# Kernel optimization log

Hardware: AMD Instinct MI355X
Metric: run time of the kernel (lower is better)

Reference implementation:

```python
import jax, jax.numpy as jnp
import numpy as np

N = 100000
E = 1000000
D_IN = 64
H1, C1 = 12, 12   # conv1: heads=12, out=12 -> concat 144
H2, C2 = 1, 64    # conv2: heads=1, out=64
NEG_SLOPE = 0.2
ALPHA = 0.5       # SSGConv alpha, K=1


def setup_inputs() -> dict:
    key = jax.random.key(0)
    ks = jax.random.split(key, 16)
    features = jax.random.normal(ks[0], (N, D_IN), dtype=jnp.float32)
    # edges with no self loops (PyG GATv2 removes then re-adds self loops)
    src = jax.random.randint(ks[1], (E,), 0, N)
    off = jax.random.randint(ks[2], (E,), 1, N)
    dst = (src + off) % N
    edge_index = jnp.stack([src, dst]).astype(jnp.int64)
    g = lambda k, shape, fan: (jax.random.normal(k, shape, jnp.float32) * (1.0 / np.sqrt(fan)))
    params = dict(
        W_ssg=g(ks[3], (D_IN, D_IN), D_IN), b_ssg=jnp.zeros((D_IN,), jnp.float32),
        W1l=g(ks[4], (D_IN, H1 * C1), D_IN), b1l=jnp.zeros((H1 * C1,), jnp.float32),
        W1r=g(ks[5], (D_IN, H1 * C1), D_IN), b1r=jnp.zeros((H1 * C1,), jnp.float32),
        att1=g(ks[6], (H1, C1), C1), bias1=jnp.zeros((H1 * C1,), jnp.float32),
        W2l=g(ks[7], (H1 * C1, H2 * C2), H1 * C1), b2l=jnp.zeros((H2 * C2,), jnp.float32),
        W2r=g(ks[8], (H1 * C1, H2 * C2), H1 * C1), b2r=jnp.zeros((H2 * C2,), jnp.float32),
        att2=g(ks[9], (H2, C2), C2), bias2=jnp.zeros((H2 * C2,), jnp.float32),
    )
    return dict(features=features, edge_index=edge_index, **params)


def _add_self_loops(src, dst):
    loop = jnp.arange(N, dtype=src.dtype)
    return jnp.concatenate([src, loop]), jnp.concatenate([dst, loop])


def _ssg_conv(x, src, dst, W, b):
    # gcn_norm with self loops, edge weight 1
    s, d = _add_self_loops(src, dst)
    deg = jax.ops.segment_sum(jnp.ones_like(s, dtype=x.dtype), d, num_segments=N)
    dinv = jnp.where(deg > 0, jax.lax.rsqrt(deg), 0.0)
    norm = dinv[s] * dinv[d]                      # [E+N]
    agg = jax.ops.segment_sum(x[s] * norm[:, None], d, num_segments=N)
    h = ALPHA * x + (1.0 - ALPHA) * agg           # K=1
    return h @ W + b


def _gatv2_conv(x, src, dst, Wl, bl, Wr, br, att, bias, Hh, Cc):
    s, d = _add_self_loops(src, dst)
    xl = (x @ Wl + bl).reshape(N, Hh, Cc)
    xr = (x @ Wr + br).reshape(N, Hh, Cc)
    e = jax.nn.leaky_relu(xl[s] + xr[d], NEG_SLOPE)       # [E', H, C]
    logits = jnp.einsum('ehc,hc->eh', e, att)             # [E', H]
    m = jax.ops.segment_max(logits, d, num_segments=N)    # [N, H]
    a = jnp.exp(logits - m[d])
    denom = jax.ops.segment_sum(a, d, num_segments=N)
    a = a / (denom[d] + 1e-16)                            # segment softmax
    out = jax.ops.segment_sum(xl[s] * a[:, :, None], d, num_segments=N)
    return out.reshape(N, Hh * Cc) + bias


def reference(features, edge_index, W_ssg, b_ssg, W1l, b1l, W1r, b1r,
              att1, bias1, W2l, b2l, W2r, b2r, att2, bias2):
    src, dst = edge_index[0], edge_index[1]
    x = _ssg_conv(features, src, dst, W_ssg, b_ssg)
    x = _gatv2_conv(x, src, dst, W1l, b1l, W1r, b1r, att1, bias1, H1, C1)
    x = _gatv2_conv(x, src, dst, W2l, b2l, W2r, b2r, att2, bias2, H2, C2)
    return x
```

## Files before the change

### kernel.cpp

```cpp
#include <hip/hip_runtime.h>

#define NNODE 100000
#define NEDGE 1000000
#define CAP 64

typedef __attribute__((ext_vector_type(4))) float f32x4;
typedef __attribute__((ext_vector_type(8))) short bf16x8;

__device__ __forceinline__ float lrelu(float x){ return x >= 0.f ? x : 0.2f*x; }
__device__ __forceinline__ unsigned short f2bf(float f){
    unsigned u = __float_as_uint(f);
    unsigned r = (u + 0x7FFFu + ((u >> 16) & 1u)) >> 16;
    return (unsigned short)r;
}
__device__ __forceinline__ float bf2f(unsigned short h){
    return __uint_as_float(((unsigned)h) << 16);
}

__global__ void detect_kernel(const int* __restrict__ ei, int* __restrict__ flag){
    int t = threadIdx.x;
    int nz = ei[2*t + 1];
    unsigned long long b = __ballot(nz != 0);
    if (t == 0) flag[0] = (b == 0ULL) ? 1 : 0;
}

__global__ __launch_bounds__(256) void scatter_kernel(const int* __restrict__ ei,
                                                      const int* __restrict__ flag,
                                                      int* __restrict__ cnt,
                                                      int* __restrict__ col){
    int e = blockIdx.x * 256 + threadIdx.x;
    if (e >= NEDGE) return;
    int s, d;
    if (flag[0]){ s = ei[2*e]; d = ei[2*(NEDGE + e)]; }
    else        { s = ei[e];   d = ei[NEDGE + e]; }
    if ((unsigned)s < NNODE && (unsigned)d < NNODE){
        int p = atomicAdd(&cnt[d], 1);
        if (p < CAP) col[d*CAP + p] = s;
    }
}

__global__ __launch_bounds__(256) void setup_kernel(const int* __restrict__ cnt,
                                                    float* __restrict__ dinv,
                                                    const float* __restrict__ Wssg,
                                                    const float* __restrict__ bssg,
                                                    const float* __restrict__ W1l,
                                                    const float* __restrict__ b1l,
                                                    const float* __restrict__ W1r,
                                                    const float* __restrict__ b1r,
                                                    unsigned short* __restrict__ Wct,
                                                    float* __restrict__ bc,
                                                    const float* __restrict__ W2l,
                                                    const float* __restrict__ b2l,
                                                    const float* __restrict__ W2r,
                                                    const float* __restrict__ b2r,
                                                    unsigned short* __restrict__ W2t,
                                                    float* __restrict__ b2c){
    int b = blockIdx.x;
    if (b < 391){
        int i = b * 256 + threadIdx.x;
        if (i < NNODE) dinv[i] = rsqrtf((float)(cnt[i] + 1));
    } else if (b < 463){
        int id = (b - 391) * 256 + threadIdx.x;
        if (id < 2*64*144){
            int which = id / (64*144);
            int rem = id - which*64*144;
            int k = rem / 144, j = rem - (rem/144)*144;
            const float* W1 = which ? W1r : W1l;
            float s = 0.f;
            #pragma unroll 8
            for (int c = 0; c < 64; ++c)
                s = fmaf(Wssg[k*64 + c], W1[c*144 + j], s);
            Wct[(size_t)(which*144 + j)*64 + k] = f2bf(s);
        }
        if (id < 2*144){
            int which = id / 144, j = id - which*144;
            const float* W1 = which ? W1r : W1l;
            const float* b1 = which ? b1r : b1l;
            float s = b1[j];
            #pragma unroll 8
            for (int c = 0; c < 64; ++c)
                s = fmaf(bssg[c], W1[c*144 + j], s);
            bc[which*144 + j] = s;
        }
    } else {
        int id = (b - 463) * 256 + threadIdx.x;
        if (id < 128*160){
            int j = id / 160, k = id - (id/160)*160;
            float v = 0.f;
            if (k < 144) v = (j < 64) ? W2l[k*64 + j] : W2r[k*64 + (j - 64)];
            W2t[(size_t)j*160 + k] = f2bf(v);
        }
        if (id < 128) b2c[id] = (id < 64) ? b2l[id] : b2r[id - 64];
    }
}

__global__ __launch_bounds__(256) void ssg_kernel(const float* __restrict__ x,
                                                  const int* __restrict__ col,
                                                  const int* __restrict__ cnt,
                                                  const float* __restrict__ dinv,
                                                  unsigned short* __restrict__ hb){
    int wid = threadIdx.x >> 6, lane = threadIdx.x & 63;
    int d = blockIdx.x * 4 + wid;
    int cq = lane & 7, eq = lane >> 3;
    float di = dinv[d];
    int deg = min(cnt[d], CAP);
    int myc = (lane < deg) ? col[d*CAP + lane] : 0;
    float wl = (lane < deg) ? dinv[myc] : 0.f;
    float a0=0.f,a1=0.f,a2=0.f,a3=0.f,a4=0.f,a5=0.f,a6=0.f,a7=0.f;
    for (int e0 = 0; e0 < deg; e0 += 8){
        int e = e0 + eq;
        bool val = e < deg;
        int idx = val ? e : 0;
        int se = __shfl(myc, idx);
        float w = __shfl(wl, idx);
        if (!val) w = 0.f;
        float4 v0 = *(const float4*)&x[(size_t)se*64 + 8*cq];
        float4 v1 = *(const float4*)&x[(size_t)se*64 + 8*cq + 4];
        a0 = fmaf(w, v0.x, a0); a1 = fmaf(w, v0.y, a1);
        a2 = fmaf(w, v0.z, a2); a3 = fmaf(w, v0.w, a3);
        a4 = fmaf(w, v1.x, a4); a5 = fmaf(w, v1.y, a5);
        a6 = fmaf(w, v1.z, a6); a7 = fmaf(w, v1.w, a7);
    }
    #pragma unroll
    for (int m = 8; m < 64; m <<= 1){
        a0 += __shfl_xor(a0, m); a1 += __shfl_xor(a1, m);
        a2 += __shfl_xor(a2, m); a3 += __shfl_xor(a3, m);
        a4 += __shfl_xor(a4, m); a5 += __shfl_xor(a5, m);
        a6 += __shfl_xor(a6, m); a7 += __shfl_xor(a7, m);
    }
    if (eq == 0){
        float4 xd0 = *(const float4*)&x[(size_t)d*64 + 8*cq];
        float4 xd1 = *(const float4*)&x[(size_t)d*64 + 8*cq + 4];
        float dd = di*di;
        ushort4 o0, o1;
        o0.x = f2bf(0.5f*xd0.x + 0.5f*fmaf(di, a0, dd*xd0.x));
        o0.y = f2bf(0.5f*xd0.y + 0.5f*fmaf(di, a1, dd*xd0.y));
        o0.z = f2bf(0.5f*xd0.z + 0.5f*fmaf(di, a2, dd*xd0.z));
        o0.w = f2bf(0.5f*xd0.w + 0.5f*fmaf(di, a3, dd*xd0.w));
        o1.x = f2bf(0.5f*xd1.x + 0.5f*fmaf(di, a4, dd*xd1.x));
        o1.y = f2bf(0.5f*xd1.y + 0.5f*fmaf(di, a5, dd*xd1.y));
        o1.z = f2bf(0.5f*xd1.z + 0.5f*fmaf(di, a6, dd*xd1.z));
        o1.w = f2bf(0.5f*xd1.w + 0.5f*fmaf(di, a7, dd*xd1.w));
        *(ushort4*)&hb[(size_t)d*64 + 8*cq]     = o0;
        *(ushort4*)&hb[(size_t)d*64 + 8*cq + 4] = o1;
    }
}

template<int K, int OUT1, int OUT2>
__global__ __launch_bounds__(256) void gemm_mfma_kernel(const unsigned short* __restrict__ Xb,
                                                        const unsigned short* __restrict__ Wt,
                                                        const float* __restrict__ Bc,
                                                        unsigned short* __restrict__ Y1,
                                                        unsigned short* __restrict__ Y2){
    constexpr int OUT = OUT1 + OUT2;
    constexpr int NT = OUT / 16;
    int wid = threadIdx.x >> 6, lane = threadIdx.x & 63;
    int m = lane & 15, kg = lane >> 4;
    int row0 = blockIdx.x * 64 + wid * 16;
    int rA = row0 + m; if (rA > NNODE-1) rA = NNODE-1;
    f32x4 acc[NT];
    #pragma unroll
    for (int t = 0; t < NT; ++t) acc[t] = (f32x4){0.f, 0.f, 0.f, 0.f};
    #pragma unroll
    for (int k0 = 0; k0 < K; k0 += 32){
        bf16x8 a = *(const bf16x8*)&Xb[(size_t)rA*K + k0 + 8*kg];
        #pragma unroll
        for (int t = 0; t < NT; ++t){
            bf16x8 b = *(const bf16x8*)&Wt[(size_t)(t*16 + m)*K + k0 + 8*kg];
            acc[t] = __builtin_amdgcn_mfma_f32_16x16x32_bf16(a, b, acc[t], 0, 0, 0);
        }
    }
    int rbase = row0 + 4*kg;
    #pragma unroll
    for (int t = 0; t < NT; ++t){
        int colg = t*16 + m;
        float bias = Bc[colg];
        #pragma unroll
        for (int r = 0; r < 4; ++r){
            int gr = rbase + r;
            if (gr < NNODE){
                unsigned short v = f2bf(acc[t][r] + bias);
                if (colg < OUT1) Y1[(size_t)gr*OUT1 + colg] = v;
                else             Y2[(size_t)gr*OUT2 + (colg - OUT1)] = v;
            }
        }
    }
}

__global__ __launch_bounds__(192) void gat1_kernel(const unsigned short* __restrict__ xl,
                                                   const unsigned short* __restrict__ xr,
                                                   const int* __restrict__ col,
                                                   const int* __restrict__ cnt,
                                                   const float* __restrict__ att,
                                                   const float* __restrict__ bias,
                                                   unsigned short* __restrict__ xg){
    __shared__ __align__(16) float V[16][148];
    __shared__ float A[16][13];
    __shared__ __align__(16) float P[4][36][4];
    __shared__ float Lp[4][12];
    __shared__ int scol[65];
    int d = blockIdx.x, t = threadIdx.x;
    int deg = min(cnt[d], CAP);
    int ne = deg + 1;
    if (t < deg) scol[t] = col[d*CAP + t];
    if (t == deg) scol[t] = d;
    int h = t % 12;
    int eslot = t / 12;
    float xrr[12], attr[12];
    {
        const ushort4* xrp = (const ushort4*)&xr[(size_t)d*144 + h*12];
        ushort4 q0 = xrp[0], q1 = xrp[1], q2 = xrp[2];
        xrr[0]=bf2f(q0.x); xrr[1]=bf2f(q0.y); xrr[2]=bf2f(q0.z); xrr[3]=bf2f(q0.w);
        xrr[4]=bf2f(q1.x); xrr[5]=bf2f(q1.y); xrr[6]=bf2f(q1.z); xrr[7]=bf2f(q1.w);
        xrr[8]=bf2f(q2.x); xrr[9]=bf2f(q2.y); xrr[10]=bf2f(q2.z); xrr[11]=bf2f(q2.w);
    }
    #pragma unroll
    for (int c = 0; c < 12; ++c) attr[c] = att[h*12 + c];
    int eg = t / 36, cg = t - (t/36)*36;
    int hc = cg / 3;
    float4 acc4 = make_float4(0.f, 0.f, 0.f, 0.f);
    float l = 0.f;
    __syncthreads();
    for (int e0 = 0; e0 < ne; e0 += 16){
        int e = e0 + eslot;
        if (e < ne){
            const ushort4* row = (const ushort4*)&xl[(size_t)scol[e]*144 + h*12];
            ushort4 q0 = row[0], q1 = row[1], q2 = row[2];
            float v0=bf2f(q0.x), v1=bf2f(q0.y), v2=bf2f(q0.z), v3=bf2f(q0.w);
            float v4=bf2f(q1.x), v5=bf2f(q1.y), v6=bf2f(q1.z), v7=bf2f(q1.w);
            float v8=bf2f(q2.x), v9=bf2f(q2.y), v10=bf2f(q2.z), v11=bf2f(q2.w);
            float s = 0.f;
            s = fmaf(lrelu(v0 + xrr[0]),  attr[0],  s);
            s = fmaf(lrelu(v1 + xrr[1]),  attr[1],  s);
            s = fmaf(lrelu(v2 + xrr[2]),  attr[2],  s);
            s = fmaf(lrelu(v3 + xrr[3]),  attr[3],  s);
            s = fmaf(lrelu(v4 + xrr[4]),  attr[4],  s);
            s = fmaf(lrelu(v5 + xrr[5]),  attr[5],  s);
            s = fmaf(lrelu(v6 + xrr[6]),  attr[6],  s);
            s = fmaf(lrelu(v7 + xrr[7]),  attr[7],  s);
            s = fmaf(lrelu(v8 + xrr[8]),  attr[8],  s);
            s = fmaf(lrelu(v9 + xrr[9]),  attr[9],  s);
            s = fmaf(lrelu(v10 + xrr[10]), attr[10], s);
            s = fmaf(lrelu(v11 + xrr[11]), attr[11], s);
            A[eslot][h] = __expf(s);
            *(float4*)&V[eslot][h*12]     = make_float4(v0, v1, v2, v3);
            *(float4*)&V[eslot][h*12 + 4] = make_float4(v4, v5, v6, v7);
            *(float4*)&V[eslot][h*12 + 8] = make_float4(v8, v9, v10, v11);
        }
        __syncthreads();
        if (t < 144){
            int lim = ne - e0; if (lim > 16) lim = 16;
            for (int ee = eg; ee < lim; ee += 4){
                float a = A[ee][hc];
                float4 v = *(const float4*)&V[ee][4*cg];
                acc4.x = fmaf(a, v.x, acc4.x);
                acc4.y = fmaf(a, v.y, acc4.y);
                acc4.z = fmaf(a, v.z, acc4.z);
                acc4.w = fmaf(a, v.w, acc4.w);
                l += a;
            }
        }
        __syncthreads();
    }
    if (t < 144){
        *(float4*)&P[eg][cg][0] = acc4;
        if (cg - hc*3 == 0) Lp[eg][hc] = l;
    }
    __syncthreads();
    if (t < 144){
        int cgf = t >> 2, cif = t & 3, hh = t / 12;
        float acc = P[0][cgf][cif] + P[1][cgf][cif] + P[2][cgf][cif] + P[3][cgf][cif];
        float ll  = Lp[0][hh] + Lp[1][hh] + Lp[2][hh] + Lp[3][hh];
        xg[(size_t)d*160 + t] = f2bf(acc / (ll + 1e-16f) + bias[t]);
    } else if (t < 160){
        xg[(size_t)d*160 + t] = 0;
    }
}

__global__ __launch_bounds__(256) void gat2_kernel(const unsigned short* __restrict__ xl,
                                                   const unsigned short* __restrict__ xr,
                                                   const int* __restrict__ col,
                                                   const int* __restrict__ cnt,
                                                   const float* __restrict__ att,
                                                   const float* __restrict__ bias,
                                                   float* __restrict__ out){
    __shared__ float V[4][8][68];
    __shared__ float Aw[4][8];
    int wid = threadIdx.x >> 6, lane = threadIdx.x & 63;
    int d0 = blockIdx.x * 4;
    int d = d0 + wid;
    int deg = min(cnt[d], 63);
    int ne = deg + 1;
    int nemax = 1;
    #pragma unroll
    for (int j = 0; j < 4; ++j) nemax = max(nemax, min(cnt[d0+j], 63) + 1);
    int eq = lane >> 3, cq = lane & 7;
    float4 xra, xrb;
    {
        ushort4 u0 = *(const ushort4*)&xr[(size_t)d*64 + 8*cq];
        ushort4 u1 = *(const ushort4*)&xr[(size_t)d*64 + 8*cq + 4];
        xra = make_float4(bf2f(u0.x), bf2f(u0.y), bf2f(u0.z), bf2f(u0.w));
        xrb = make_float4(bf2f(u1.x), bf2f(u1.y), bf2f(u1.z), bf2f(u1.w));
    }
    float4 ata = *(const float4*)&att[8*cq];
    float4 atb = *(const float4*)&att[8*cq + 4];
    int myc = (lane < deg) ? col[d*CAP + lane] : d;
    float acc = 0.f, l = 0.f;
    for (int e0 = 0; e0 < nemax; e0 += 8){
        int e = e0 + eq;
        bool val = (e < ne);
        int se = __shfl(myc, val ? e : 0);
        float4 va = make_float4(0.f,0.f,0.f,0.f), vb = va;
        if (val){
            ushort4 u0 = *(const ushort4*)&xl[(size_t)se*64 + 8*cq];
            ushort4 u1 = *(const ushort4*)&xl[(size_t)se*64 + 8*cq + 4];
            va = make_float4(bf2f(u0.x), bf2f(u0.y), bf2f(u0.z), bf2f(u0.w));
            vb = make_float4(bf2f(u1.x), bf2f(u1.y), bf2f(u1.z), bf2f(u1.w));
        }
        float part = 0.f;
        part = fmaf(lrelu(va.x + xra.x), ata.x, part);
        part = fmaf(lrelu(va.y + xra.y), ata.y, part);
        part = fmaf(lrelu(va.z + xra.z), ata.z, part);
        part = fmaf(lrelu(va.w + xra.w), ata.w, part);
        part = fmaf(lrelu(vb.x + xrb.x), atb.x, part);
        part = fmaf(lrelu(vb.y + xrb.y), atb.y, part);
        part = fmaf(lrelu(vb.z + xrb.z), atb.z, part);
        part = fmaf(lrelu(vb.w + xrb.w), atb.w, part);
        part += __shfl_xor(part, 1);
        part += __shfl_xor(part, 2);
        part += __shfl_xor(part, 4);
        *(float4*)&V[wid][eq][8*cq]     = va;
        *(float4*)&V[wid][eq][8*cq + 4] = vb;
        if (cq == 0) Aw[wid][eq] = val ? __expf(part) : 0.f;
        __syncthreads();
        int lim = ne - e0; if (lim > 8) lim = 8;
        for (int j = 0; j < lim; ++j){
            float a = Aw[wid][j];
            l += a;
            acc = fmaf(a, V[wid][j][lane], acc);
        }
        __syncthreads();
    }
    out[(size_t)d*64 + lane] = acc / (l + 1e-16f) + bias[lane];
}

extern "C" void kernel_launch(void* const* d_in, const int* in_sizes, int n_in,
                              void* d_out, int out_size, void* d_ws, size_t ws_size,
                              hipStream_t stream){
    const float* feat  = (const float*)d_in[0];
    const int*   ei    = (const int*)d_in[1];
    const float* W_ssg = (const float*)d_in[2];
    const float* b_ssg = (const float*)d_in[3];
    const float* W1l   = (const float*)d_in[4];
    const float* b1l   = (const float*)d_in[5];
    const float* W1r   = (const float*)d_in[6];
    const float* b1r   = (const float*)d_in[7];
    const float* att1  = (const float*)d_in[8];
    const float* bias1 = (const float*)d_in[9];
    const float* W2l   = (const float*)d_in[10];
    const float* b2l   = (const float*)d_in[11];
    const float* W2r   = (const float*)d_in[12];
    const float* b2r   = (const float*)d_in[13];
    const float* att2  = (const float*)d_in[14];
    const float* bias2 = (const float*)d_in[15];
    float* out = (float*)d_out;

    char* ws = (char*)d_ws;
    size_t off = 0;
    auto alloc = [&](size_t bytes)->void*{
        void* p = ws + off; off = (off + bytes + 255) & ~(size_t)255; return p;
    };
    int*            flag = (int*)           alloc(4);
    int*            cnt  = (int*)           alloc((size_t)NNODE*4);
    int*            col  = (int*)           alloc((size_t)NNODE*CAP*4);
    float*          dinv = (float*)         alloc((size_t)NNODE*4);
    unsigned short* hb   = (unsigned short*)alloc((size_t)NNODE*64*2);
    unsigned short* xl1b = (unsigned short*)alloc((size_t)NNODE*144*2);
    unsigned short* xr1b = (unsigned short*)alloc((size_t)NNODE*144*2);
    unsigned short* xg   = (unsigned short*)alloc((size_t)NNODE*160*2);
    unsigned short* xl2b = (unsigned short*)alloc((size_t)NNODE*64*2);
    unsigned short* xr2b = (unsigned short*)alloc((size_t)NNODE*64*2);
    unsigned short* Wct  = (unsigned short*)alloc((size_t)288*64*2);
    float*          bc   = (float*)         alloc((size_t)288*4);
    unsigned short* W2t  = (unsigned short*)alloc((size_t)128*160*2);
    float*          b2c  = (float*)         alloc((size_t)128*4);

    hipMemsetAsync(cnt, 0, (size_t)NNODE*4, stream);
    detect_kernel<<<1, 64, 0, stream>>>(ei, flag);
    scatter_kernel<<<(NEDGE + 255)/256, 256, 0, stream>>>(ei, flag, cnt, col);
    setup_kernel<<<543, 256, 0, stream>>>(cnt, dinv,
                                          W_ssg, b_ssg, W1l, b1l, W1r, b1r, Wct, bc,
                                          W2l, b2l, W2r, b2r, W2t, b2c);

    ssg_kernel<<<NNODE/4, 256, 0, stream>>>(feat, col, cnt, dinv, hb);

    gemm_mfma_kernel<64,144,144><<<1563, 256, 0, stream>>>(hb, Wct, bc, xl1b, xr1b);

    gat1_kernel<<<NNODE, 192, 0, stream>>>(xl1b, xr1b, col, cnt, att1, bias1, xg);

    gemm_mfma_kernel<160,64,64><<<1563, 256, 0, stream>>>(xg, W2t, b2c, xl2b, xr2b);

    gat2_kernel<<<NNODE/4, 256, 0, stream>>>(xl2b, xr2b, col, cnt, att2, bias2, out);
}
```

Measured before the change: 495.7 us.

## Gather bf16 copy of features in SSG and simplify GAT1 accumulation

Fuses into the scatter kernel a conversion of the input features to a bf16 copy. The SSG neighbor gather then reads that copy, halving the bytes fetched per random row access. Separately, the GAT1 aggregation drops the 4-way edge-group split with float4 partial sums and the shared-memory reduction. Each of 144 threads now loops over all edges for one channel. This trades fewer reduction steps and barriers for a longer serial loop per thread, and the bf16 gather adds some rounding error to SSG.

```diff
diff --git a/kernel.cpp b/kernel.cpp
--- a/kernel.cpp
+++ b/kernel.cpp
@@ -27,15 +27,30 @@
 __global__ __launch_bounds__(256) void scatter_kernel(const int* __restrict__ ei,
                                                       const int* __restrict__ flag,
                                                       int* __restrict__ cnt,
-                                                      int* __restrict__ col){
-    int e = blockIdx.x * 256 + threadIdx.x;
-    if (e >= NEDGE) return;
-    int s, d;
-    if (flag[0]){ s = ei[2*e]; d = ei[2*(NEDGE + e)]; }
-    else        { s = ei[e];   d = ei[NEDGE + e]; }
-    if ((unsigned)s < NNODE && (unsigned)d < NNODE){
-        int p = atomicAdd(&cnt[d], 1);
-        if (p < CAP) col[d*CAP + p] = s;
+                                                      int* __restrict__ col,
+                                                      const float* __restrict__ x,
+                                                      unsigned short* __restrict__ xb){
+    int gid = blockIdx.x * 256 + threadIdx.x;
+    if (gid < NEDGE){
+        int s, d;
+        if (flag[0]){ s = ei[2*gid]; d = ei[2*(NEDGE + gid)]; }
+        else        { s = ei[gid];   d = ei[NEDGE + gid]; }
+        if ((unsigned)s < NNODE && (unsigned)d < NNODE){
+            int p = atomicAdd(&cnt[d], 1);
+            if (p < CAP) col[d*CAP + p] = s;
+        }
+        return;
+    }
+    int cid = gid - NEDGE;
+    if (cid < NNODE*8){
+        int d = cid >> 3, c8 = (cid & 7) * 8;
+        float4 v0 = *(const float4*)&x[(size_t)d*64 + c8];
+        float4 v1 = *(const float4*)&x[(size_t)d*64 + c8 + 4];
+        ushort4 o0, o1;
+        o0.x = f2bf(v0.x); o0.y = f2bf(v0.y); o0.z = f2bf(v0.z); o0.w = f2bf(v0.w);
+        o1.x = f2bf(v1.x); o1.y = f2bf(v1.y); o1.z = f2bf(v1.z); o1.w = f2bf(v1.w);
+        *(ushort4*)&xb[(size_t)d*64 + c8]     = o0;
+        *(ushort4*)&xb[(size_t)d*64 + c8 + 4] = o1;
     }
 }
 
@@ -95,6 +110,7 @@
 }
 
 __global__ __launch_bounds__(256) void ssg_kernel(const float* __restrict__ x,
+                                                  const unsigned short* __restrict__ xb,
                                                   const int* __restrict__ col,
                                                   const int* __restrict__ cnt,
                                                   const float* __restrict__ dinv,
@@ -114,12 +130,12 @@
         int se = __shfl(myc, idx);
         float w = __shfl(wl, idx);
         if (!val) w = 0.f;
-        float4 v0 = *(const float4*)&x[(size_t)se*64 + 8*cq];
-        float4 v1 = *(const float4*)&x[(size_t)se*64 + 8*cq + 4];
-        a0 = fmaf(w, v0.x, a0); a1 = fmaf(w, v0.y, a1);
-        a2 = fmaf(w, v0.z, a2); a3 = fmaf(w, v0.w, a3);
-        a4 = fmaf(w, v1.x, a4); a5 = fmaf(w, v1.y, a5);
-        a6 = fmaf(w, v1.z, a6); a7 = fmaf(w, v1.w, a7);
+        ushort4 u0 = *(const ushort4*)&xb[(size_t)se*64 + 8*cq];
+        ushort4 u1 = *(const ushort4*)&xb[(size_t)se*64 + 8*cq + 4];
+        a0 = fmaf(w, bf2f(u0.x), a0); a1 = fmaf(w, bf2f(u0.y), a1);
+        a2 = fmaf(w, bf2f(u0.z), a2); a3 = fmaf(w, bf2f(u0.w), a3);
+        a4 = fmaf(w, bf2f(u1.x), a4); a5 = fmaf(w, bf2f(u1.y), a5);
+        a6 = fmaf(w, bf2f(u1.z), a6); a7 = fmaf(w, bf2f(u1.w), a7);
     }
     #pragma unroll
     for (int m = 8; m < 64; m <<= 1){
@@ -196,8 +212,6 @@
                                                    unsigned short* __restrict__ xg){
     __shared__ __align__(16) float V[16][148];
     __shared__ float A[16][13];
-    __shared__ __align__(16) float P[4][36][4];
-    __shared__ float Lp[4][12];
     __shared__ int scol[65];
     int d = blockIdx.x, t = threadIdx.x;
     int deg = min(cnt[d], CAP);
@@ -216,10 +230,8 @@
     }
     #pragma unroll
     for (int c = 0; c < 12; ++c) attr[c] = att[h*12 + c];
-    int eg = t / 36, cg = t - (t/36)*36;
-    int hc = cg / 3;
-    float4 acc4 = make_float4(0.f, 0.f, 0.f, 0.f);
-    float l = 0.f;
+    int hh = t / 12;
+    float acc = 0.f, l = 0.f;
     __syncthreads();
     for (int e0 = 0; e0 < ne; e0 += 16){
         int e = e0 + eslot;
@@ -250,31 +262,17 @@
         __syncthreads();
         if (t < 144){
             int lim = ne - e0; if (lim > 16) lim = 16;
-            for (int ee = eg; ee < lim; ee += 4){
-                float a = A[ee][hc];
-                float4 v = *(const float4*)&V[ee][4*cg];
-                acc4.x = fmaf(a, v.x, acc4.x);
-                acc4.y = fmaf(a, v.y, acc4.y);
-                acc4.z = fmaf(a, v.z, acc4.z);
-                acc4.w = fmaf(a, v.w, acc4.w);
+            for (int ee = 0; ee < lim; ++ee){
+                float a  = A[ee][hh];
+                float xv = V[ee][t];
                 l += a;
+                acc = fmaf(a, xv, acc);
             }
         }
         __syncthreads();
     }
-    if (t < 144){
-        *(float4*)&P[eg][cg][0] = acc4;
-        if (cg - hc*3 == 0) Lp[eg][hc] = l;
-    }
-    __syncthreads();
-    if (t < 144){
-        int cgf = t >> 2, cif = t & 3, hh = t / 12;
-        float acc = P[0][cgf][cif] + P[1][cgf][cif] + P[2][cgf][cif] + P[3][cgf][cif];
-        float ll  = Lp[0][hh] + Lp[1][hh] + Lp[2][hh] + Lp[3][hh];
-        xg[(size_t)d*160 + t] = f2bf(acc / (ll + 1e-16f) + bias[t]);
-    } else if (t < 160){
-        xg[(size_t)d*160 + t] = 0;
-    }
+    if (t < 144) xg[(size_t)d*160 + t] = f2bf(acc / (l + 1e-16f) + bias[t]);
+    else if (t < 160) xg[(size_t)d*160 + t] = 0;
 }
 
 __global__ __launch_bounds__(256) void gat2_kernel(const unsigned short* __restrict__ xl,
@@ -374,6 +372,7 @@
     int*            cnt  = (int*)           alloc((size_t)NNODE*4);
     int*            col  = (int*)           alloc((size_t)NNODE*CAP*4);
     float*          dinv = (float*)         alloc((size_t)NNODE*4);
+    unsigned short* xb   = (unsigned short*)alloc((size_t)NNODE*64*2);
     unsigned short* hb   = (unsigned short*)alloc((size_t)NNODE*64*2);
     unsigned short* xl1b = (unsigned short*)alloc((size_t)NNODE*144*2);
     unsigned short* xr1b = (unsigned short*)alloc((size_t)NNODE*144*2);
@@ -387,12 +386,13 @@
 
     hipMemsetAsync(cnt, 0, (size_t)NNODE*4, stream);
     detect_kernel<<<1, 64, 0, stream>>>(ei, flag);
-    scatter_kernel<<<(NEDGE + 255)/256, 256, 0, stream>>>(ei, flag, cnt, col);
+    scatter_kernel<<<(NEDGE + NNODE*8 + 255)/256, 256, 0, stream>>>(ei, flag, cnt, col,
+                                                                    feat, xb);
     setup_kernel<<<543, 256, 0, stream>>>(cnt, dinv,
                                           W_ssg, b_ssg, W1l, b1l, W1r, b1r, Wct, bc,
                                           W2l, b2l, W2r, b2r, W2t, b2c);
 
-    ssg_kernel<<<NNODE/4, 256, 0, stream>>>(feat, col, cnt, dinv, hb);
+    ssg_kernel<<<NNODE/4, 256, 0, stream>>>(feat, xb, col, cnt, dinv, hb);
 
     gemm_mfma_kernel<64,144,144><<<1563, 256, 0, stream>>>(hb, Wct, bc, xl1b, xr1b);
 
```

After: 498.9 us. Within noise of the previous version (+0.6%).
